# Performance work log

Measured on AMD Instinct MI355X. Metric: run time of the kernel, lower is better.

The kernel has to match this reference:

```python
import jax, jax.numpy as jnp
import numpy as np

N_CUST, N_PROD, D, H, OUT, E = 100000, 10000, 128, 128, 64, 500000
RELS = ["purchase", "redeem", "transfer_to", "transfer_from", "dividend_from"]


def setup_inputs() -> dict:
    key = jax.random.key(0)
    ks = jax.random.split(key, 40)
    inp = {}
    inp["x_cust"] = jax.random.normal(ks[0], (N_CUST, D), jnp.float32)
    inp["x_prod"] = jax.random.normal(ks[1], (N_PROD, D), jnp.float32)
    for i, r in enumerate(RELS):
        inp["src_" + r] = jax.random.randint(ks[2 + 2 * i], (E,), 0, N_CUST)
        inp["dst_" + r] = jax.random.randint(ks[3 + 2 * i], (E,), 0, N_PROD)
    s = 0.05
    names = [("W_gcn", (D, H)), ("b_gcn", (H,)), ("Ws_gat", (D, H)), ("Wd_gat", (D, H)),
             ("a_s_gat", (H,)), ("a_d_gat", (H,)), ("b_gat", (H,)),
             ("Wl_to", (D, H)), ("b_to", (H,)), ("Wr_to", (D, H)),
             ("Wl_from", (D, H)), ("b_from", (H,)), ("Wr_from", (D, H)),
             ("Wl_div", (D, H)), ("b_div", (H,)), ("Wr_div", (D, H)),
             ("W_out", (H, OUT)), ("b_out", (OUT,))]
    for i, (n, shp) in enumerate(names):
        inp[n] = jax.random.normal(ks[12 + i], shp, jnp.float32) * s
    return inp


def _gcn(x_src, src, dst, W, b):
    # symmetric-norm bipartite GCN: transform then gather->scale->scatter
    deg_s = jax.ops.segment_sum(jnp.ones_like(src, jnp.float32), src, N_CUST)
    deg_d = jax.ops.segment_sum(jnp.ones_like(dst, jnp.float32), dst, N_PROD)
    norm = jax.lax.rsqrt(deg_s[src] * deg_d[dst])  # [E]
    h = x_src @ W  # [N_CUST, H]
    return jax.ops.segment_sum(norm[:, None] * h[src], dst, N_PROD) + b


def _gat(x_src, x_dst, src, dst, Ws, Wd, a_s, a_d, b):
    # single-head bipartite GAT with edge-softmax over incoming edges at dst
    hs = x_src @ Ws                     # [N_CUST, H]
    ls = hs @ a_s                       # [N_CUST]
    ld = (x_dst @ Wd) @ a_d             # [N_PROD]
    logit = jax.nn.leaky_relu(ls[src] + ld[dst], 0.2)  # [E]
    m = jax.ops.segment_max(logit, dst, N_PROD)
    e = jnp.exp(logit - m[dst])
    den = jax.ops.segment_sum(e, dst, N_PROD)
    alpha = e / den[dst]
    return jax.ops.segment_sum(alpha[:, None] * hs[src], dst, N_PROD) + b


def _sage(x_src, x_dst, src, dst, Wl, bl, Wr):
    # mean-aggregate raw src features, then linear; plus root transform of dst
    s = jax.ops.segment_sum(x_src[src], dst, N_PROD)
    c = jax.ops.segment_sum(jnp.ones_like(dst, jnp.float32), dst, N_PROD)
    mean = s / jnp.maximum(c, 1.0)[:, None]
    return mean @ Wl + bl + x_dst @ Wr


def reference(x_cust, x_prod, src_purchase, dst_purchase, src_redeem, dst_redeem,
              src_transfer_to, dst_transfer_to, src_transfer_from, dst_transfer_from,
              src_dividend_from, dst_dividend_from,
              W_gcn, b_gcn, Ws_gat, Wd_gat, a_s_gat, a_d_gat, b_gat,
              Wl_to, b_to, Wr_to, Wl_from, b_from, Wr_from, Wl_div, b_div, Wr_div,
              W_out, b_out):
    prod = _gcn(x_cust, src_purchase, dst_purchase, W_gcn, b_gcn)
    prod = prod + _gat(x_cust, x_prod, src_redeem, dst_redeem, Ws_gat, Wd_gat, a_s_gat, a_d_gat, b_gat)
    prod = prod + _sage(x_cust, x_prod, src_transfer_to, dst_transfer_to, Wl_to, b_to, Wr_to)
    prod = prod + _sage(x_cust, x_prod, src_transfer_from, dst_transfer_from, Wl_from, b_from, Wr_from)
    prod = prod + _sage(x_cust, x_prod, src_dividend_from, dst_dividend_from, Wl_div, b_div, Wr_div)
    prod = jax.nn.relu(prod)  # HeteroConv(aggr='sum') then relu
    return prod @ W_out + b_out  # [N_PROD, OUT]
```

## Files before the change

kernel.cpp:

```cpp
#include <hip/hip_runtime.h>

#define WF 64
#define CAP 128
#define CH 2048
#define LC 32
#define NGMAX 160
#define BINCAP 3584

typedef int v4i __attribute__((ext_vector_type(4)));
typedef short short8 __attribute__((ext_vector_type(8)));
typedef short s16x4 __attribute__((ext_vector_type(4)));
typedef float f32x4 __attribute__((ext_vector_type(4)));
typedef float f32x2 __attribute__((ext_vector_type(2)));

#if __has_builtin(__builtin_amdgcn_cvt_f32_fp8) && __has_builtin(__builtin_amdgcn_cvt_pk_fp8_f32)
#define HW_FP8 1
#endif

__device__ __forceinline__ unsigned fp8enc1(float x) {
    unsigned b = __builtin_bit_cast(unsigned, x);
    unsigned s = (b >> 24) & 0x80u;
    int E = (b >> 23) & 0xff;
    unsigned m = b & 0x7fffffu;
    unsigned mr = (m + 0x7ffffu + ((m >> 20) & 1u)) >> 20;
    int e8 = E - 120 + (int)(mr >> 3);
    mr &= 7u;
    if (e8 <= 0) return s;
    if (e8 > 15) { e8 = 15; mr = 7u; }
    return s | ((unsigned)e8 << 3) | mr;
}
__device__ __forceinline__ float fp8dec1(unsigned u8) {
    unsigned f = ((u8 & 0x80u) << 24) | (((u8 & 0x7fu) << 20) + 0x3C000000u);
    return (u8 & 0x7fu) ? __builtin_bit_cast(float, f) : 0.f;
}
__device__ __forceinline__ unsigned fp8pack4(float4 u) {
#ifdef HW_FP8
    int r = __builtin_amdgcn_cvt_pk_fp8_f32(u.x, u.y, 0, false);
    r = __builtin_amdgcn_cvt_pk_fp8_f32(u.z, u.w, r, true);
    return (unsigned)r;
#else
    return fp8enc1(u.x) | (fp8enc1(u.y) << 8) | (fp8enc1(u.z) << 16) | (fp8enc1(u.w) << 24);
#endif
}
__device__ __forceinline__ void accP2(float w, unsigned u, f32x2& A, f32x2& B) {
    f32x2 w2 = {w, w};
#if defined(HW_FP8) && __has_builtin(__builtin_amdgcn_cvt_pk_f32_fp8)
    f32x2 d0 = __builtin_amdgcn_cvt_pk_f32_fp8((int)u, false);
    f32x2 d1 = __builtin_amdgcn_cvt_pk_f32_fp8((int)u, true);
    A = __builtin_elementwise_fma(w2, d0, A);
    B = __builtin_elementwise_fma(w2, d1, B);
#elif defined(HW_FP8)
    f32x2 d0 = {__builtin_amdgcn_cvt_f32_fp8((int)u, 0), __builtin_amdgcn_cvt_f32_fp8((int)u, 1)};
    f32x2 d1 = {__builtin_amdgcn_cvt_f32_fp8((int)u, 2), __builtin_amdgcn_cvt_f32_fp8((int)u, 3)};
    A = __builtin_elementwise_fma(w2, d0, A);
    B = __builtin_elementwise_fma(w2, d1, B);
#else
    A[0] = fmaf(w, fp8dec1(u & 0xffu), A[0]);
    A[1] = fmaf(w, fp8dec1((u >> 8) & 0xffu), A[1]);
    B[0] = fmaf(w, fp8dec1((u >> 16) & 0xffu), B[0]);
    B[1] = fmaf(w, fp8dec1(u >> 24), B[1]);
#endif
}

__device__ __forceinline__ short bf16r(float x) {
    unsigned u = __builtin_bit_cast(unsigned, x);
    u += 0x7fffu + ((u >> 16) & 1u);
    return (short)(u >> 16);
}
__device__ __forceinline__ void bfsplit(float x, short& hi, short& lo) {
    unsigned u = __builtin_bit_cast(unsigned, x);
    hi = (short)(u >> 16);
    float fh = __builtin_bit_cast(float, u & 0xffff0000u);
    lo = bf16r(x - fh);
}

__global__ void k_init(int* deg_s, int nc2, int* bincur, int nb, int ZB,
                       const float* __restrict__ Ws, const float* __restrict__ Wd,
                       const float* __restrict__ as_, const float* __restrict__ ad_,
                       const float* __restrict__ bg, const float* __restrict__ bga,
                       const float* __restrict__ bto, const float* __restrict__ bfr,
                       const float* __restrict__ bdv,
                       const float* __restrict__ Wg, const float* __restrict__ Wlt,
                       const float* __restrict__ Wlf, const float* __restrict__ Wld,
                       const float* __restrict__ Wrt, const float* __restrict__ Wrf,
                       const float* __restrict__ Wrd, const float* __restrict__ Wo,
                       float* vs, float* vd, float* bsum,
                       short* wth, short* wtl, short* woth, short* wotl) {
    int b = blockIdx.x, t = threadIdx.x;
    if (b < ZB) {
        int i = b * 256 + t;
        if (i < nc2) deg_s[i] = 0;
        if (i < nb) bincur[i] = 0;
    } else if (b == ZB) {
        if (t < 128) {
            float a = 0.f, bb = 0.f;
            for (int h = 0; h < 128; ++h) {
                a += Ws[t * 128 + h] * as_[h];
                bb += Wd[t * 128 + h] * ad_[h];
            }
            vs[t] = a; vd[t] = bb;
            bsum[t] = bg[t] + bga[t] + bto[t] + bfr[t] + bdv[t];
        }
    } else if (b < ZB + 385) {
        int e = (b - ZB - 1) * 256 + t;
        int h = e / 768;
        int q = e - h * 768;
        int m = q >> 7, k = q & 127;
        int src = k * 128 + h;
        float val;
        switch (m) {
            case 0: val = Wg[src]; break;
            case 1: val = Ws[src]; break;
            case 2: val = Wlt[src]; break;
            case 3: val = Wlf[src]; break;
            case 4: val = Wld[src]; break;
            default: val = Wrt[src] + Wrf[src] + Wrd[src]; break;
        }
        short hi, lo;
        bfsplit(val, hi, lo);
        wth[e] = hi; wtl[e] = lo;
    } else {
        int e = (b - ZB - 385) * 256 + t;
        int o = e >> 7, k = e & 127;
        short hi, lo;
        bfsplit(Wo[k * 64 + o], hi, lo);
        woth[e] = hi; wotl[e] = lo;
    }
}

__global__ __launch_bounds__(256) void k_bin(
    const int* s0, const int* s1, const int* s2, const int* s3, const int* s4,
    const int* d0, const int* d1, const int* d2, const int* d3, const int* d4,
    int* bincur, int* gbin, int* deg_s, int E, int NP, int ng,
    int bpjE, int B0, int HB4, int CB,
    const float* __restrict__ xc, const float* __restrict__ xp,
    const float* __restrict__ vs, const float* __restrict__ vd,
    unsigned* __restrict__ xh, float* __restrict__ lsb, float* __restrict__ ldb,
    short* __restrict__ xph, short* __restrict__ xpl, int NC) {
    __shared__ int lcnt[NGMAX];
    __shared__ int lbase[NGMAX];
    __shared__ int lbin[NGMAX * LC];
    int b = blockIdx.x, t = threadIdx.x;
    if (b < B0) {
        int rel = b / bpjE;
        int blk = b - rel * bpjE;
        const int *sp, *dp;
        switch (rel) {
            case 0: sp = s0; dp = d0; break;
            case 1: sp = s1; dp = d1; break;
            case 2: sp = s2; dp = d2; break;
            case 3: sp = s3; dp = d3; break;
            default: sp = s4; dp = d4; break;
        }
        for (int i = t; i < ng; i += 256) lcnt[i] = 0;
        __syncthreads();
        int* bc = bincur + rel * ng;
        int* gb0 = gbin + (size_t)rel * ng * BINCAP;
        int start = blk * CH;
        int q0 = start + t * 8;
#pragma unroll
        for (int c = 0; c < 8; c += 4) {
            int q = q0 + c;
            if (q >= E) break;
            if (q + 3 < E) {
                v4i dv = __builtin_nontemporal_load((const v4i*)(dp + q));
                v4i sv = __builtin_nontemporal_load((const v4i*)(sp + q));
                int dd[4] = {dv.x, dv.y, dv.z, dv.w};
                int ss[4] = {sv.x, sv.y, sv.z, sv.w};
#pragma unroll
                for (int z = 0; z < 4; ++z) {
                    int bin = dd[z] >> 6;
                    int pk = (ss[z] << 6) | (dd[z] & 63);
                    int pos = atomicAdd(&lcnt[bin], 1);
                    if (pos < LC) lbin[bin * LC + pos] = pk;
                    else {
                        int g = atomicAdd(bc + bin, 1);
                        if (g < BINCAP) gb0[(size_t)bin * BINCAP + g] = pk;
                    }
                }
            } else {
                for (int i = q; i < E; ++i) {
                    int d = dp[i];
                    int bin = d >> 6;
                    int pk = (sp[i] << 6) | (d & 63);
                    int pos = atomicAdd(&lcnt[bin], 1);
                    if (pos < LC) lbin[bin * LC + pos] = pk;
                    else {
                        int g = atomicAdd(bc + bin, 1);
                        if (g < BINCAP) gb0[(size_t)bin * BINCAP + g] = pk;
                    }
                }
            }
        }
        __syncthreads();
        if (t < ng) {
            int c = min(lcnt[t], LC);
            lbase[t] = atomicAdd(bc + t, c);
        }
        __syncthreads();
        int wv = t >> 6, lane = t & 63;
        for (int bin = wv; bin < ng; bin += 4) {
            int c = min(lcnt[bin], LC);
            int gbase = lbase[bin];
            int* gp = gb0 + (size_t)bin * BINCAP;
            for (int i = lane; i < c; i += 64) {
                int g = gbase + i;
                if (g < BINCAP) gp[g] = lbin[bin * LC + i];
            }
        }
    } else if (b < B0 + HB4) {
        int q = ((b - B0) * 256 + t) * 4;
        if (q >= E) return;
        if (q + 3 < E) {
            v4i v = __builtin_nontemporal_load((const v4i*)(s0 + q));
            atomicAdd(deg_s + v.x, 1); atomicAdd(deg_s + v.y, 1);
            atomicAdd(deg_s + v.z, 1); atomicAdd(deg_s + v.w, 1);
        } else {
            for (int i = q; i < E; ++i) atomicAdd(deg_s + s0[i], 1);
        }
    } else if (b < B0 + HB4 + CB) {
        int row = (b - B0 - HB4) * 8 + (t >> 5);
        int q = t & 31;
        if (row >= NC) return;
        float4 u = *(const float4*)(xc + (size_t)row * 128 + 4 * q);
        float4 v = *(const float4*)(vs + 4 * q);
        float s = u.x * v.x + u.y * v.y + u.z * v.z + u.w * v.w;
        xh[(size_t)row * 32 + q] = fp8pack4(u);
#pragma unroll
        for (int o = 16; o; o >>= 1) s += __shfl_xor(s, o, WF);
        if (q == 0) lsb[row] = s;
    } else {
        int row = (b - B0 - HB4 - CB) * 4 + (t >> 6);
        int l = t & 63;
        if (row >= NP) return;
        const float* xr = xp + (size_t)row * 128;
        float x0 = xr[2 * l], x1 = xr[2 * l + 1];
        short h0, lo0, h1, lo1;
        bfsplit(x0, h0, lo0);
        bfsplit(x1, h1, lo1);
        ((unsigned*)(xph + (size_t)row * 128))[l] =
            (unsigned)(unsigned short)h0 | ((unsigned)(unsigned short)h1 << 16);
        ((unsigned*)(xpl + (size_t)row * 128))[l] =
            (unsigned)(unsigned short)lo0 | ((unsigned)(unsigned short)lo1 << 16);
        float s = x0 * vd[2 * l] + x1 * vd[2 * l + 1];
        for (int o = 32; o; o >>= 1) s += __shfl_down(s, o, WF);
        if (l == 0) ldb[row] = s;
    }
}

__global__ __launch_bounds__(256) void k_aggf(
    const int* __restrict__ gbin, const int* __restrict__ bincur,
    const int* __restrict__ deg_s,
    const float* __restrict__ ls, const float* __restrict__ ld,
    const unsigned* __restrict__ xh,
    short* __restrict__ aggH, short* __restrict__ aggL,
    int NP, int ng) {
    __shared__ int cnt[16];
    __shared__ int buck[16][CAP + 4];
    __shared__ float wbuf[4][CAP + 4];
    int t = threadIdx.x;
    int rel = blockIdx.x / (4 * ng);
    int rem = blockIdx.x - rel * 4 * ng;
    int grp = rem >> 2, sub = rem & 3;
    if (t < 16) cnt[t] = 0;
    __syncthreads();
    int binid = rel * ng + grp;
    int n = min(bincur[binid], BINCAP);
    const int* bsrc = gbin + (size_t)binid * BINCAP;
    for (int i = t; i < n; i += 256) {
        int e = bsrc[i];
        int lp = e & 63;
        if ((lp >> 4) == sub) {
            int li = lp & 15;
            int pos = atomicAdd(&cnt[li], 1);
            if (pos < CAP) buck[li][pos] = e >> 6;
        }
    }
    __syncthreads();
    if (t < 16) {
        int c = min(cnt[t], CAP);
        buck[t][c] = 0; buck[t][c + 1] = 0; buck[t][c + 2] = 0;
    }
    __syncthreads();

    int wv = t >> 6, l = t & 63;
    int g = l >> 4, q8 = l & 15;

    for (int r = 0; r < 4; ++r) {
        int li = r * 4 + wv;
        int p = grp * 64 + sub * 16 + li;
        bool valid = (p < NP);
        int m = valid ? min(cnt[li], CAP) : 0;

        if (rel == 0) {
            float rd = rsqrtf((float)m);
            for (int e = l; e < m; e += WF)
                wbuf[wv][e] = rsqrtf((float)deg_s[buck[li][e]]) * rd;
        } else if (rel == 1) {
            if (m > 0) {
                float ldp = ld[p];
                float ml = -3.4e38f, dl = 0.f;
                for (int e = l; e < m; e += WF) {
                    float tt = ls[buck[li][e]] + ldp;
                    tt = tt > 0.f ? tt : 0.2f * tt;
                    wbuf[wv][e] = tt;
                    if (tt > ml) { dl = dl * __expf(ml - tt) + 1.f; ml = tt; }
                    else dl += __expf(tt - ml);
                }
                for (int o = 32; o; o >>= 1) {
                    float m2 = __shfl_xor(ml, o, WF), d2 = __shfl_xor(dl, o, WF);
                    float mm = fmaxf(ml, m2);
                    dl = dl * __expf(ml - mm) + d2 * __expf(m2 - mm);
                    ml = mm;
                }
                float inv = 1.f / dl;
                for (int e = l; e < m; e += WF)
                    wbuf[wv][e] = __expf(wbuf[wv][e] - ml) * inv;
            }
        } else {
            float sc = 1.f / fmaxf((float)m, 1.f);
            for (int e = l; e < m; e += WF) wbuf[wv][e] = sc;
        }
        if (l == 0) { wbuf[wv][m] = 0.f; wbuf[wv][m + 1] = 0.f; wbuf[wv][m + 2] = 0.f; }
        __builtin_amdgcn_wave_barrier();

        f32x2 a0 = {0.f, 0.f}, a1 = {0.f, 0.f}, a2 = {0.f, 0.f}, a3 = {0.f, 0.f};
        int nq = (m + 3) >> 2;
        int j = 0;
        for (; j + 4 <= nq; j += 4) {
            int ss[4]; float wk[4]; uint2 uu[4];
#pragma unroll
            for (int z = 0; z < 4; ++z) {
                int e = 4 * (j + z) + g;
                ss[z] = buck[li][e];
                wk[z] = wbuf[wv][e];
            }
#pragma unroll
            for (int z = 0; z < 4; ++z)
                uu[z] = *(const uint2*)(xh + (size_t)ss[z] * 32 + 2 * q8);
#pragma unroll
            for (int z = 0; z < 4; ++z) {
                accP2(wk[z], uu[z].x, a0, a1);
                accP2(wk[z], uu[z].y, a2, a3);
            }
        }
        for (; j < nq; ++j) {
            int e = 4 * j + g;
            int s0 = buck[li][e];
            float w0 = wbuf[wv][e];
            uint2 u0 = *(const uint2*)(xh + (size_t)s0 * 32 + 2 * q8);
            accP2(w0, u0.x, a0, a1);
            accP2(w0, u0.y, a2, a3);
        }

#pragma unroll
        for (int o = 16; o <= 32; o <<= 1) {
            a0[0] += __shfl_xor(a0[0], o, WF); a0[1] += __shfl_xor(a0[1], o, WF);
            a1[0] += __shfl_xor(a1[0], o, WF); a1[1] += __shfl_xor(a1[1], o, WF);
            a2[0] += __shfl_xor(a2[0], o, WF); a2[1] += __shfl_xor(a2[1], o, WF);
            a3[0] += __shfl_xor(a3[0], o, WF); a3[1] += __shfl_xor(a3[1], o, WF);
        }

        if (valid && l < 16) {
            short8 hv, lv;
            short hh, ll;
            bfsplit(a0[0], hh, ll); hv[0] = hh; lv[0] = ll;
            bfsplit(a0[1], hh, ll); hv[1] = hh; lv[1] = ll;
            bfsplit(a1[0], hh, ll); hv[2] = hh; lv[2] = ll;
            bfsplit(a1[1], hh, ll); hv[3] = hh; lv[3] = ll;
            bfsplit(a2[0], hh, ll); hv[4] = hh; lv[4] = ll;
            bfsplit(a2[1], hh, ll); hv[5] = hh; lv[5] = ll;
            bfsplit(a3[0], hh, ll); hv[6] = hh; lv[6] = ll;
            bfsplit(a3[1], hh, ll); hv[7] = hh; lv[7] = ll;
            size_t base = ((size_t)rel * NP + p) * 128 + 8 * q8;
            *(short8*)(aggH + base) = hv;
            *(short8*)(aggL + base) = lv;
        }
    }
}

__global__ __launch_bounds__(256, 2) void k_gemm_out(
    const short* __restrict__ aggH, const short* __restrict__ aggL,
    const short* __restrict__ wth, const short* __restrict__ wtl,
    const short* __restrict__ woth, const short* __restrict__ wotl,
    const float* __restrict__ bsum, const float* __restrict__ bout,
    float* __restrict__ out, int NP) {
    __shared__ short c1h[16][136];
    __shared__ short c1l[16][136];
    int t = threadIdx.x;
    int w = t >> 6, l = t & 63;
    int lr = l & 15, lq = l >> 4;
    int kq = lq * 8;
    int row0 = blockIdx.x * 16;
    int ar = row0 + lr;
    if (ar > NP - 1) ar = NP - 1;

    f32x4 acc[2] = {};

#pragma unroll
    for (int m = 0; m < 6; ++m) {
        const short* ahp = aggH + ((size_t)m * NP + ar) * 128;
        const short* alp = aggL + ((size_t)m * NP + ar) * 128;
#pragma unroll
        for (int kk = 0; kk < 4; ++kk) {
            int ko = kk * 32 + kq;
            short8 ah = *(const short8*)(ahp + ko);
            short8 al = *(const short8*)(alp + ko);
            int kbase = m * 128 + ko;
#pragma unroll
            for (int ci = 0; ci < 2; ++ci) {
                int hcol = 32 * w + 16 * ci + lr;
                short8 bh = *(const short8*)(wth + (size_t)hcol * 768 + kbase);
                short8 bl = *(const short8*)(wtl + (size_t)hcol * 768 + kbase);
                acc[ci] = __builtin_amdgcn_mfma_f32_16x16x32_bf16(ah, bh, acc[ci], 0, 0, 0);
                acc[ci] = __builtin_amdgcn_mfma_f32_16x16x32_bf16(al, bh, acc[ci], 0, 0, 0);
                acc[ci] = __builtin_amdgcn_mfma_f32_16x16x32_bf16(ah, bl, acc[ci], 0, 0, 0);
            }
        }
    }

#pragma unroll
    for (int ci = 0; ci < 2; ++ci) {
        int col = 32 * w + 16 * ci + lr;
        float bs = bsum[col];
#pragma unroll
        for (int r = 0; r < 4; ++r) {
            float v = acc[ci][r] + bs;
            v = v > 0.f ? v : 0.f;
            short hh, ll;
            bfsplit(v, hh, ll);
            int rl = 4 * lq + r;
            c1h[rl][col] = hh;
            c1l[rl][col] = ll;
        }
    }
    __syncthreads();

    f32x4 acc2 = {};
#pragma unroll
    for (int kb = 0; kb < 4; ++kb) {
        int kof = kb * 32 + kq;
        short8 a2h = *(const short8*)&c1h[lr][kof];
        short8 a2l = *(const short8*)&c1l[lr][kof];
        int o = 16 * w + lr;
        short8 b2h = *(const short8*)(woth + o * 128 + kof);
        short8 b2l = *(const short8*)(wotl + o * 128 + kof);
        acc2 = __builtin_amdgcn_mfma_f32_16x16x32_bf16(a2h, b2h, acc2, 0, 0, 0);
        acc2 = __builtin_amdgcn_mfma_f32_16x16x32_bf16(a2l, b2h, acc2, 0, 0, 0);
        acc2 = __builtin_amdgcn_mfma_f32_16x16x32_bf16(a2h, b2l, acc2, 0, 0, 0);
    }
    int col = 16 * w + lr;
    float bo = bout[col];
#pragma unroll
    for (int r = 0; r < 4; ++r) {
        int row = row0 + 4 * lq + r;
        if (row < NP) out[(size_t)row * 64 + col] = acc2[r] + bo;
    }
}

extern "C" void kernel_launch(void* const* d_in, const int* in_sizes, int n_in,
                              void* d_out, int out_size, void* d_ws, size_t ws_size,
                              hipStream_t stream) {
    const float* x_cust = (const float*)d_in[0];
    const float* x_prod = (const float*)d_in[1];
    const int* src_pur = (const int*)d_in[2];  const int* dst_pur = (const int*)d_in[3];
    const int* src_red = (const int*)d_in[4];  const int* dst_red = (const int*)d_in[5];
    const int* src_to  = (const int*)d_in[6];  const int* dst_to  = (const int*)d_in[7];
    const int* src_fr  = (const int*)d_in[8];  const int* dst_fr  = (const int*)d_in[9];
    const int* src_dv  = (const int*)d_in[10]; const int* dst_dv  = (const int*)d_in[11];
    const float* W_gcn = (const float*)d_in[12];
    const float* b_gcn = (const float*)d_in[13];
    const float* Ws_gat = (const float*)d_in[14]; const float* Wd_gat = (const float*)d_in[15];
    const float* a_s = (const float*)d_in[16]; const float* a_d = (const float*)d_in[17];
    const float* b_gat = (const float*)d_in[18];
    const float* Wl_to = (const float*)d_in[19]; const float* b_to = (const float*)d_in[20];
    const float* Wr_to = (const float*)d_in[21];
    const float* Wl_fr = (const float*)d_in[22]; const float* b_fr = (const float*)d_in[23];
    const float* Wr_fr = (const float*)d_in[24];
    const float* Wl_dv = (const float*)d_in[25]; const float* b_dv = (const float*)d_in[26];
    const float* Wr_dv = (const float*)d_in[27];
    const float* W_out = (const float*)d_in[28]; const float* b_out = (const float*)d_in[29];
    float* out = (float*)d_out;

    int NC = in_sizes[0] / 128;
    int NP = in_sizes[1] / 128;
    int E  = in_sizes[2];
    int ng = (NP + 63) >> 6;

    char* ws = (char*)d_ws;
    size_t off = 0;
    auto alloc = [&](size_t bytes) -> void* {
        void* p = ws + off;
        off = (off + bytes + 255) & ~(size_t)255;
        return p;
    };
    int*      deg_s  = (int*)alloc((size_t)NC * 4);
    int*      bincur = (int*)alloc((size_t)5 * NGMAX * 4);
    int*      gbin   = (int*)alloc((size_t)5 * NGMAX * BINCAP * 4);
    float*    lsb    = (float*)alloc((size_t)NC * 4);
    float*    ldb    = (float*)alloc((size_t)NP * 4);
    float*    vs     = (float*)alloc(512);
    float*    vd     = (float*)alloc(512);
    float*    bsum   = (float*)alloc(512);
    short*    wth    = (short*)alloc((size_t)98304 * 2);
    short*    wtl    = (short*)alloc((size_t)98304 * 2);
    short*    woth   = (short*)alloc((size_t)8192 * 2);
    short*    wotl   = (short*)alloc((size_t)8192 * 2);
    unsigned* xh     = (unsigned*)alloc((size_t)NC * 32 * 4);
    short*    aggH   = (short*)alloc((size_t)6 * NP * 128 * 2);
    short*    aggL   = (short*)alloc((size_t)6 * NP * 128 * 2);
    short*    xph    = aggH + (size_t)5 * NP * 128;
    short*    xpl    = aggL + (size_t)5 * NP * 128;

    int ZB = (NC + 255) / 256;
    k_init<<<ZB + 1 + 384 + 32, 256, 0, stream>>>(deg_s, NC, bincur, 5 * ng, ZB,
                                                  Ws_gat, Wd_gat, a_s, a_d,
                                                  b_gcn, b_gat, b_to, b_fr, b_dv,
                                                  W_gcn, Wl_to, Wl_fr, Wl_dv,
                                                  Wr_to, Wr_fr, Wr_dv, W_out,
                                                  vs, vd, bsum, wth, wtl, woth, wotl);

    int bpjE = (E + CH - 1) / CH;
    int bpj4 = ((E + 3) / 4 + 255) / 256;
    int B0 = 5 * bpjE, HB4 = bpj4, CB = (NC + 7) / 8, PB = (NP + 3) / 4;
    k_bin<<<B0 + HB4 + CB + PB, 256, 0, stream>>>(
        src_pur, src_red, src_to, src_fr, src_dv,
        dst_pur, dst_red, dst_to, dst_fr, dst_dv,
        bincur, gbin, deg_s, E, NP, ng, bpjE, B0, HB4, CB,
        x_cust, x_prod, vs, vd, xh, lsb, ldb, xph, xpl, NC);

    k_aggf<<<5 * ng * 4, 256, 0, stream>>>(gbin, bincur, deg_s, lsb, ldb, xh,
                                           aggH, aggL, NP, ng);

    k_gemm_out<<<(NP + 15) / 16, 256, 0, stream>>>(
        aggH, aggL, wth, wtl, woth, wotl, bsum, b_out, out, NP);
}
```

Measured before the change: 297.6 us.

## Stage GEMM weight slices in swizzled LDS via global_load_lds

In k_gemm_out, each 128x128 hi/lo weight slice per relation is now copied into shared memory with direct global-to-LDS loads, and MFMA B operands are read from LDS instead of global memory. The weight layout is written XOR-swizzled in the prep kernel so the LDS reads avoid bank conflicts. This targets repeated global/L2 weight fetches by every block, but it adds 64KB of LDS per block, which likely limits occupancy, plus two barriers per relation.

```diff
diff --git a/kernel.cpp b/kernel.cpp
--- a/kernel.cpp
+++ b/kernel.cpp
@@ -9,13 +9,18 @@
 
 typedef int v4i __attribute__((ext_vector_type(4)));
 typedef short short8 __attribute__((ext_vector_type(8)));
-typedef short s16x4 __attribute__((ext_vector_type(4)));
 typedef float f32x4 __attribute__((ext_vector_type(4)));
 typedef float f32x2 __attribute__((ext_vector_type(2)));
 
 #if __has_builtin(__builtin_amdgcn_cvt_f32_fp8) && __has_builtin(__builtin_amdgcn_cvt_pk_fp8_f32)
 #define HW_FP8 1
 #endif
+
+__device__ __forceinline__ void gload_lds16(const void* g, void* lds) {
+    __builtin_amdgcn_global_load_lds(
+        (const __attribute__((address_space(1))) unsigned int*)g,
+        (__attribute__((address_space(3))) unsigned int*)lds, 16, 0, 0);
+}
 
 __device__ __forceinline__ unsigned fp8enc1(float x) {
     unsigned b = __builtin_bit_cast(unsigned, x);
@@ -118,7 +123,9 @@
         }
         short hi, lo;
         bfsplit(val, hi, lo);
-        wth[e] = hi; wtl[e] = lo;
+        int kswz = k ^ ((h & 7) << 3);
+        int idx = h * 768 + m * 128 + kswz;
+        wth[idx] = hi; wtl[idx] = lo;
     } else {
         int e = (b - ZB - 385) * 256 + t;
         int o = e >> 7, k = e & 127;
@@ -385,6 +392,8 @@
     const short* __restrict__ woth, const short* __restrict__ wotl,
     const float* __restrict__ bsum, const float* __restrict__ bout,
     float* __restrict__ out, int NP) {
+    __shared__ short bsh[128 * 128];
+    __shared__ short bsl[128 * 128];
     __shared__ short c1h[16][136];
     __shared__ short c1l[16][136];
     int t = threadIdx.x;
@@ -395,10 +404,33 @@
     int ar = row0 + lr;
     if (ar > NP - 1) ar = NP - 1;
 
+    int srow = w * 4;
+    int lbyte = 0;
+    (void)lbyte;
+
     f32x4 acc[2] = {};
 
 #pragma unroll
     for (int m = 0; m < 6; ++m) {
+        __syncthreads();
+        {
+            const char* srch = (const char*)wth + m * 256;
+            const char* srcl = (const char*)wtl + m * 256;
+            int hb = srow + (l >> 4);
+            int cb = (l & 15) * 16;
+#pragma unroll
+            for (int i = 0; i < 8; ++i) {
+                int h = i * 16 + hb;
+                gload_lds16(srch + h * 1536 + cb, (char*)bsh + (i * 16 + srow) * 256);
+            }
+#pragma unroll
+            for (int i = 0; i < 8; ++i) {
+                int h = i * 16 + hb;
+                gload_lds16(srcl + h * 1536 + cb, (char*)bsl + (i * 16 + srow) * 256);
+            }
+        }
+        __syncthreads();
+
         const short* ahp = aggH + ((size_t)m * NP + ar) * 128;
         const short* alp = aggL + ((size_t)m * NP + ar) * 128;
 #pragma unroll
@@ -406,12 +438,12 @@
             int ko = kk * 32 + kq;
             short8 ah = *(const short8*)(ahp + ko);
             short8 al = *(const short8*)(alp + ko);
-            int kbase = m * 128 + ko;
 #pragma unroll
             for (int ci = 0; ci < 2; ++ci) {
                 int hcol = 32 * w + 16 * ci + lr;
-                short8 bh = *(const short8*)(wth + (size_t)hcol * 768 + kbase);
-                short8 bl = *(const short8*)(wtl + (size_t)hcol * 768 + kbase);
+                int boff = hcol * 256 + ((ko * 2) ^ ((hcol & 7) << 4));
+                short8 bh = *(const short8*)((const char*)bsh + boff);
+                short8 bl = *(const short8*)((const char*)bsl + boff);
                 acc[ci] = __builtin_amdgcn_mfma_f32_16x16x32_bf16(ah, bh, acc[ci], 0, 0, 0);
                 acc[ci] = __builtin_amdgcn_mfma_f32_16x16x32_bf16(al, bh, acc[ci], 0, 0, 0);
                 acc[ci] = __builtin_amdgcn_mfma_f32_16x16x32_bf16(ah, bl, acc[ci], 0, 0, 0);
```

Result: faster. 280.9 us (-5.6%).
